# Performance work log

Measured on AMD Instinct MI355X. Metric: run time of the kernel, lower is better.

Reference implementation:

```python
import jax, jax.numpy as jnp
import numpy as np

N_ENTITY = 500000
N_RELATION = 1000
EMB = 128
BATCH = 131072


def setup_inputs() -> dict:
    key = jax.random.key(0)
    k_h, k_r, k_t, k_e, k_rel = jax.random.split(key, 5)
    head = jax.random.randint(k_h, (BATCH,), 0, N_ENTITY)
    rel = jax.random.randint(k_r, (BATCH,), 0, N_RELATION)
    tail = jax.random.randint(k_t, (BATCH,), 0, N_ENTITY)
    triple = jnp.stack([head, rel, tail], axis=1)  # [B,3] int
    # init_weights: uniform(-0.1, 0.1) for embeddings
    entity_emb = jax.random.uniform(k_e, (N_ENTITY, EMB), jnp.float32, -0.1, 0.1)
    relation_emb = jax.random.uniform(k_rel, (N_RELATION, EMB), jnp.float32, -0.1, 0.1)
    De = jnp.eye(EMB, dtype=jnp.float32)
    Dr = jnp.eye(EMB, dtype=jnp.float32)
    b_c = jnp.zeros((BATCH, EMB), dtype=jnp.float32)
    return {"triple": triple, "entity_emb": entity_emb, "relation_emb": relation_emb,
            "De": De, "Dr": Dr, "b_c": b_c}


def reference(triple, entity_emb, relation_emb, De, Dr, b_c):
    # flag == 0 path (default): combine head+relation, score against tail
    h = entity_emb[triple[:, 0]]        # [B,E] gather
    r = relation_emb[triple[:, 1]]      # [B,E] gather
    t = entity_emb[triple[:, 2]]        # [B,E] gather
    f = jnp.tanh(h @ De + r @ Dr + b_c)  # [B,E]
    score = jnp.sum(f * t, axis=1, keepdims=True)  # vectorized per-row dot -> [B,1]
    return jax.nn.sigmoid(score)
```

## Files before the change

kernel.cpp:

```cpp
#include <hip/hip_runtime.h>

#define EMB 128
#define BM 128
#define THREADS 512

typedef __attribute__((ext_vector_type(8))) short bf16x8;
typedef __attribute__((ext_vector_type(4))) float f32x4;
typedef unsigned short u16;

__device__ __forceinline__ u16 f2bf(float f) {
    unsigned u = __builtin_bit_cast(unsigned, f);
    u += 0x7fffu + ((u >> 16) & 1u);
    return (u16)(u >> 16);
}

__global__ void setup_kernel(const float* __restrict__ rel,
                             const float* __restrict__ Dr,
                             const float* __restrict__ De,
                             float* __restrict__ Rp,
                             u16* __restrict__ Bimg, int nrel) {
    const int blk = blockIdx.x;
    if (blk < 500) {
        const int n = threadIdx.x & 127;
        const int j = blk * 2 + (threadIdx.x >> 7);
        if (j >= nrel) return;
        float a = 0.f;
        for (int k = 0; k < EMB; ++k)
            a = fmaf(rel[(size_t)j * EMB + k], Dr[(size_t)k * EMB + n], a);
        Rp[(size_t)j * EMB + n] = a;
    } else {
        const int idx  = (blk - 500) * 256 + threadIdx.x;
        const int e    = idx & 7;
        const int lane = (idx >> 3) & 63;
        const int frag = idx >> 9;
        const int ni = frag & 7, kk = frag >> 3;
        const int k = kk * 32 + (lane >> 4) * 8 + e;
        const int n = ni * 16 + (lane & 15);
        Bimg[idx] = f2bf(De[(size_t)k * EMB + n]);
    }
}

__global__ __launch_bounds__(THREADS, 4)
void projE_main(const int* __restrict__ triple,
                const float* __restrict__ ent,
                const float* __restrict__ bc,
                const float* __restrict__ Rp,
                const u16* __restrict__ Bimg,
                float* __restrict__ out)
{
    const int tid  = threadIdx.x;
    const int lane = tid & 63;
    const int w    = tid >> 6;
    const int l15  = lane & 15;
    const int l4   = lane >> 4;
    const int bm0  = blockIdx.x * BM;

    const int g    = bm0 + w * 16 + l15;
    const int hidx = triple[g * 3 + 0];
    const int ridx = triple[g * 3 + 1];
    const int tidx = triple[g * 3 + 2];

    const float* hp = ent + (size_t)hidx * EMB;
    const float* tp = ent + (size_t)tidx * EMB;

    float4 hv[8];
    #pragma unroll
    for (int kk = 0; kk < 4; ++kk) {
        hv[2 * kk]     = *reinterpret_cast<const float4*>(hp + kk * 32 + 8 * l4);
        hv[2 * kk + 1] = *reinterpret_cast<const float4*>(hp + kk * 32 + 8 * l4 + 4);
    }

    float4 tv[8];
    #pragma unroll
    for (int ci = 0; ci < 8; ++ci)
        tv[ci] = *reinterpret_cast<const float4*>(tp + ci * 16 + 4 * l4);

    bf16x8 hf[4];
    #pragma unroll
    for (int kk = 0; kk < 4; ++kk) {
        bf16x8 v;
        v[0] = (short)f2bf(hv[2 * kk].x);
        v[1] = (short)f2bf(hv[2 * kk].y);
        v[2] = (short)f2bf(hv[2 * kk].z);
        v[3] = (short)f2bf(hv[2 * kk].w);
        v[4] = (short)f2bf(hv[2 * kk + 1].x);
        v[5] = (short)f2bf(hv[2 * kk + 1].y);
        v[6] = (short)f2bf(hv[2 * kk + 1].z);
        v[7] = (short)f2bf(hv[2 * kk + 1].w);
        hf[kk] = v;
    }

    f32x4 acc[8];
    #pragma unroll
    for (int ci = 0; ci < 8; ++ci) acc[ci] = (f32x4){0.f, 0.f, 0.f, 0.f};

    #pragma unroll
    for (int kk = 0; kk < 4; ++kk) {
        #pragma unroll
        for (int ci = 0; ci < 8; ++ci) {
            const bf16x8 d = *reinterpret_cast<const bf16x8*>(
                Bimg + (((kk * 8 + ci) << 6) + lane) * 8);
            acc[ci] = __builtin_amdgcn_mfma_f32_16x16x32_bf16(d, hf[kk], acc[ci], 0, 0, 0);
        }
    }

    const float* rp = Rp + (size_t)ridx * EMB;
    const float* bp = bc + (size_t)g    * EMB;

    float dot = 0.f;
    #pragma unroll
    for (int ci = 0; ci < 8; ++ci) {
        const int col = ci * 16 + 4 * l4;
        const float4 r4 = *reinterpret_cast<const float4*>(rp + col);
        const float4 b4 = *reinterpret_cast<const float4*>(bp + col);
        #pragma unroll
        for (int e = 0; e < 4; ++e) {
            const float x  = acc[ci][e] + (&r4.x)[e] + (&b4.x)[e];
            const float e2 = __expf(2.f * x);
            const float fv = 1.f - __fdividef(2.f, e2 + 1.f);
            dot = fmaf(fv, (&tv[ci].x)[e], dot);
        }
    }
    dot += __shfl_xor(dot, 16);
    dot += __shfl_xor(dot, 32);
    if (lane < 16) out[g] = __fdividef(1.f, 1.f + __expf(-dot));
}

extern "C" void kernel_launch(void* const* d_in, const int* in_sizes, int n_in,
                              void* d_out, int out_size, void* d_ws, size_t ws_size,
                              hipStream_t stream) {
    const int*   triple = (const int*)  d_in[0];
    const float* ent    = (const float*)d_in[1];
    const float* rel    = (const float*)d_in[2];
    const float* De     = (const float*)d_in[3];
    const float* Dr     = (const float*)d_in[4];
    const float* bc     = (const float*)d_in[5];
    float* out = (float*)d_out;

    const int batch = in_sizes[0] / 3;
    const int nrel  = in_sizes[2] / EMB;

    float* Rp = (float*)d_ws;
    u16* Bimg = (u16*)((char*)d_ws + 524288);

    setup_kernel<<<dim3(564), dim3(256), 0, stream>>>(rel, Dr, De, Rp, Bimg, nrel);
    projE_main<<<dim3(batch / BM), dim3(THREADS), 0, stream>>>(triple, ent, bc, Rp, Bimg, out);
}
```

Before: 56.21 us.

## Split output columns across wave pairs and shrink blocks to raise occupancy

Each 16-row tile is now handled by two waves, each computing half of the 128 output columns, with partial dot products combined through shared memory. Blocks shrink to 32 rows and 256 threads, and the launch bound asks for 8 blocks per CU. Tail loads move into the epilogue and head loads into the k-loop, which lowers register pressure and raises occupancy and memory-level parallelism for the gathers. The cost is a __syncthreads, a shared-memory reduction, and the head row being loaded twice per row.

```diff
diff --git a/kernel.cpp b/kernel.cpp
--- a/kernel.cpp
+++ b/kernel.cpp
@@ -1,8 +1,8 @@
 #include <hip/hip_runtime.h>
 
 #define EMB 128
-#define BM 128
-#define THREADS 512
+#define BM 32
+#define THREADS 256
 
 typedef __attribute__((ext_vector_type(8))) short bf16x8;
 typedef __attribute__((ext_vector_type(4))) float f32x4;
@@ -33,14 +33,14 @@
         const int e    = idx & 7;
         const int lane = (idx >> 3) & 63;
         const int frag = idx >> 9;
-        const int ni = frag & 7, kk = frag >> 3;
+        const int ci = frag & 7, kk = frag >> 3;
         const int k = kk * 32 + (lane >> 4) * 8 + e;
-        const int n = ni * 16 + (lane & 15);
+        const int n = ci * 16 + (lane & 15);
         Bimg[idx] = f2bf(De[(size_t)k * EMB + n]);
     }
 }
 
-__global__ __launch_bounds__(THREADS, 4)
+__global__ __launch_bounds__(THREADS, 8)
 void projE_main(const int* __restrict__ triple,
                 const float* __restrict__ ent,
                 const float* __restrict__ bc,
@@ -48,82 +48,70 @@
                 const u16* __restrict__ Bimg,
                 float* __restrict__ out)
 {
+    __shared__ float part[4][16];
+
     const int tid  = threadIdx.x;
     const int lane = tid & 63;
     const int w    = tid >> 6;
     const int l15  = lane & 15;
     const int l4   = lane >> 4;
+    const int ch   = w & 1;
     const int bm0  = blockIdx.x * BM;
+    const int g    = bm0 + (w >> 1) * 16 + l15;
 
-    const int g    = bm0 + w * 16 + l15;
     const int hidx = triple[g * 3 + 0];
     const int ridx = triple[g * 3 + 1];
     const int tidx = triple[g * 3 + 2];
+    const float* hp = ent + (size_t)hidx * EMB;
 
-    const float* hp = ent + (size_t)hidx * EMB;
-    const float* tp = ent + (size_t)tidx * EMB;
-
-    float4 hv[8];
+    f32x4 acc[4];
     #pragma unroll
-    for (int kk = 0; kk < 4; ++kk) {
-        hv[2 * kk]     = *reinterpret_cast<const float4*>(hp + kk * 32 + 8 * l4);
-        hv[2 * kk + 1] = *reinterpret_cast<const float4*>(hp + kk * 32 + 8 * l4 + 4);
-    }
-
-    float4 tv[8];
-    #pragma unroll
-    for (int ci = 0; ci < 8; ++ci)
-        tv[ci] = *reinterpret_cast<const float4*>(tp + ci * 16 + 4 * l4);
-
-    bf16x8 hf[4];
-    #pragma unroll
-    for (int kk = 0; kk < 4; ++kk) {
-        bf16x8 v;
-        v[0] = (short)f2bf(hv[2 * kk].x);
-        v[1] = (short)f2bf(hv[2 * kk].y);
-        v[2] = (short)f2bf(hv[2 * kk].z);
-        v[3] = (short)f2bf(hv[2 * kk].w);
-        v[4] = (short)f2bf(hv[2 * kk + 1].x);
-        v[5] = (short)f2bf(hv[2 * kk + 1].y);
-        v[6] = (short)f2bf(hv[2 * kk + 1].z);
-        v[7] = (short)f2bf(hv[2 * kk + 1].w);
-        hf[kk] = v;
-    }
-
-    f32x4 acc[8];
-    #pragma unroll
-    for (int ci = 0; ci < 8; ++ci) acc[ci] = (f32x4){0.f, 0.f, 0.f, 0.f};
+    for (int ci = 0; ci < 4; ++ci) acc[ci] = (f32x4){0.f, 0.f, 0.f, 0.f};
 
     #pragma unroll
     for (int kk = 0; kk < 4; ++kk) {
+        const float4 a0 = *reinterpret_cast<const float4*>(hp + kk * 32 + 8 * l4);
+        const float4 a1 = *reinterpret_cast<const float4*>(hp + kk * 32 + 8 * l4 + 4);
+        bf16x8 hfrag;
+        hfrag[0] = (short)f2bf(a0.x); hfrag[1] = (short)f2bf(a0.y);
+        hfrag[2] = (short)f2bf(a0.z); hfrag[3] = (short)f2bf(a0.w);
+        hfrag[4] = (short)f2bf(a1.x); hfrag[5] = (short)f2bf(a1.y);
+        hfrag[6] = (short)f2bf(a1.z); hfrag[7] = (short)f2bf(a1.w);
         #pragma unroll
-        for (int ci = 0; ci < 8; ++ci) {
+        for (int ci = 0; ci < 4; ++ci) {
             const bf16x8 d = *reinterpret_cast<const bf16x8*>(
-                Bimg + (((kk * 8 + ci) << 6) + lane) * 8);
-            acc[ci] = __builtin_amdgcn_mfma_f32_16x16x32_bf16(d, hf[kk], acc[ci], 0, 0, 0);
+                Bimg + (((kk * 8 + ch * 4 + ci) << 6) | lane) * 8);
+            acc[ci] = __builtin_amdgcn_mfma_f32_16x16x32_bf16(d, hfrag, acc[ci], 0, 0, 0);
         }
     }
 
-    const float* rp = Rp + (size_t)ridx * EMB;
-    const float* bp = bc + (size_t)g    * EMB;
+    const float* rp = Rp  + (size_t)ridx * EMB + ch * 64;
+    const float* bp = bc  + (size_t)g    * EMB + ch * 64;
+    const float* tp = ent + (size_t)tidx * EMB + ch * 64;
 
     float dot = 0.f;
     #pragma unroll
-    for (int ci = 0; ci < 8; ++ci) {
+    for (int ci = 0; ci < 4; ++ci) {
         const int col = ci * 16 + 4 * l4;
         const float4 r4 = *reinterpret_cast<const float4*>(rp + col);
         const float4 b4 = *reinterpret_cast<const float4*>(bp + col);
+        const float4 t4 = *reinterpret_cast<const float4*>(tp + col);
         #pragma unroll
         for (int e = 0; e < 4; ++e) {
             const float x  = acc[ci][e] + (&r4.x)[e] + (&b4.x)[e];
             const float e2 = __expf(2.f * x);
             const float fv = 1.f - __fdividef(2.f, e2 + 1.f);
-            dot = fmaf(fv, (&tv[ci].x)[e], dot);
+            dot = fmaf(fv, (&t4.x)[e], dot);
         }
     }
     dot += __shfl_xor(dot, 16);
     dot += __shfl_xor(dot, 32);
-    if (lane < 16) out[g] = __fdividef(1.f, 1.f + __expf(-dot));
+    if (lane < 16) part[w][l15] = dot;
+    __syncthreads();
+    if (ch == 0 && lane < 16) {
+        const float tot = part[w][l15] + part[w + 1][l15];
+        out[g] = __fdividef(1.f, 1.f + __expf(-tot));
+    }
 }
 
 extern "C" void kernel_launch(void* const* d_in, const int* in_sizes, int n_in,
```

Result: slower. 61.17 us (+8.8%).
